# Kernel optimization log

Measured on AMD Instinct MI355X. Metric: run time of the kernel, lower is better.

The kernel has to match this reference:

```python
import jax, jax.numpy as jnp
import numpy as np

Z_NUM_LIST = [[1,1]]*12 + [[2,1]] + [[2,2]]*11 + [[4,2]] + [[4,4]]*11  # 36 layers
Z_DIM, IN_SZ, OUT_SZ, FS = 64, 16, 16, 3
N_Z = sum(o*i for o, i in Z_NUM_LIST)  # 242
_OFFS = np.concatenate([[0], np.cumsum([o*i for o, i in Z_NUM_LIST])]).astype(int)
BN_EPS = 1e-5


def setup_inputs() -> dict:
    key = jax.random.key(0)
    ks = jax.random.split(key, 8)
    x = jax.random.normal(ks[0], (1024, 3, 32, 32), dtype=jnp.float32)
    conv_w = jax.random.normal(ks[1], (16, 3, 3, 3), dtype=jnp.float32) * 0.1
    conv_b = jnp.zeros((16,), dtype=jnp.float32)
    bn_gamma = jnp.ones((16,), dtype=jnp.float32)
    bn_beta = jnp.zeros((16,), dtype=jnp.float32)
    z_all = jax.random.normal(ks[2], (N_Z, Z_DIM), dtype=jnp.float32)  # 242 z-vectors
    # HyperNet params: z -> (in_sz*z_dim), reshape (in_sz, z_dim), -> (in_sz, out_sz*f*f)
    w2 = jax.random.normal(ks[3], (Z_DIM, IN_SZ * Z_DIM), dtype=jnp.float32) * 0.125
    b2 = jnp.zeros((IN_SZ * Z_DIM,), dtype=jnp.float32)
    w1 = jax.random.normal(ks[4], (Z_DIM, OUT_SZ * FS * FS), dtype=jnp.float32) * 0.125
    b1 = jnp.zeros((OUT_SZ * FS * FS,), dtype=jnp.float32)
    return {"x": x, "conv_w": conv_w, "conv_b": conv_b, "bn_gamma": bn_gamma,
            "bn_beta": bn_beta, "z_all": z_all, "w1": w1, "b1": b1, "w2": w2, "b2": b2}


def _hypernet_batched(z_all, w1, b1, w2, b2):
    # All 242 tiny per-z MLPs as one stacked GEMM pair.
    h_in = (z_all @ w2 + b2).reshape(-1, IN_SZ, Z_DIM)          # [N, 16, 64]
    h_fin = jnp.einsum('nid,do->nio', h_in, w1) + b1            # [N, 16, 144]
    return h_fin.reshape(-1, OUT_SZ, IN_SZ, FS, FS)             # torch .view semantics


def _assemble_weights(kernels):
    # Replicates nested torch.cat(dim=1) then cat(dim=0) per Embedding.
    weights = []
    for li, (o_n, i_n) in enumerate(Z_NUM_LIST):
        k = kernels[_OFFS[li]:_OFFS[li + 1]].reshape(o_n, i_n, OUT_SZ, IN_SZ, FS, FS)
        w = k.transpose(0, 2, 1, 3, 4, 5).reshape(o_n * OUT_SZ, i_n * IN_SZ, FS, FS)
        weights.append(w)
    return weights


def reference(x, conv_w, conv_b, bn_gamma, bn_beta, z_all, w1, b1, w2, b2):
    # conv1 (3->16, 3x3, pad 1)
    y = jax.lax.conv_general_dilated(x, conv_w, (1, 1), 'SAME',
                                     dimension_numbers=('NCHW', 'OIHW', 'NCHW'))
    y = y + conv_b[None, :, None, None]
    # batchnorm (training mode: batch statistics) + relu
    mean = jnp.mean(y, axis=(0, 2, 3))
    var = jnp.var(y, axis=(0, 2, 3))
    y = (y - mean[None, :, None, None]) * jax.lax.rsqrt(var + BN_EPS)[None, :, None, None]
    y = jax.nn.relu(y * bn_gamma[None, :, None, None] + bn_beta[None, :, None, None])
    # hypernetwork weight generation (36 conv weight tensors)
    kernels = _hypernet_batched(z_all, w1, b1, w2, b2)
    weights = _assemble_weights(kernels)
    return (*weights, y)
```

## Files before the change

### kernel.cpp

```cpp
#include <hip/hip_runtime.h>

#define N_Z     242
#define W_ELEMS (N_Z * 2304)
#define NHW_F   1048576.0f

__constant__ int c_offs[37] = {0,1,2,3,4,5,6,7,8,9,10,11,12,14,18,22,26,30,34,38,
                               42,46,50,54,58,66,82,98,114,130,146,162,178,194,210,226,242};
__constant__ int c_isz[36] = {1,1,1,1,1,1,1,1,1,1,1,1, 1, 2,2,2,2,2,2,2,2,2,2,2, 2,
                              4,4,4,4,4,4,4,4,4,4,4};

template<int CTRL, int RMASK>
__device__ __forceinline__ float dpp_add(float x) {
    int s = __builtin_amdgcn_update_dpp(0, __float_as_int(x), CTRL, RMASK, 0xF, true);
    return x + __int_as_float(s);
}
__device__ __forceinline__ float wave_sum64(float x) {
    x = dpp_add<0x111, 0xF>(x);
    x = dpp_add<0x112, 0xF>(x);
    x = dpp_add<0x114, 0xF>(x);
    x = dpp_add<0x118, 0xF>(x);
    x = dpp_add<0x142, 0xA>(x);
    x = dpp_add<0x143, 0xC>(x);
    return x;
}

__device__ __forceinline__ void stage_x(const float* __restrict__ xp,
                                        float (*xs)[34][35], int t)
{
    for (int idx = t; idx < 3 * 34 * 35; idx += 256) {
        const int ci  = idx / 1190;
        const int rem = idx - ci * 1190;
        const int rr  = rem / 35, cc = rem - rr * 35;
        float v = 0.0f;
        if (rr >= 1 && rr <= 32 && cc >= 1 && cc <= 32)
            v = xp[ci * 1024 + (rr - 1) * 32 + (cc - 1)];
        xs[ci][rr][cc] = v;
    }
}

__device__ __forceinline__ void load_window(const float (*xs)[34][35],
                                            float xv[3][3][6], int h, int w0)
{
    #pragma unroll
    for (int ci = 0; ci < 3; ++ci)
        #pragma unroll
        for (int rr = 0; rr < 3; ++rr)
            #pragma unroll
            for (int j = 0; j < 6; ++j)
                xv[ci][rr][j] = xs[ci][h + rr][w0 + j];
}

union Smem1 {
    struct { float zsh[64]; float hin[1024]; } h;
    struct { float xs[3][34][35]; float red[4][32]; } c;
};

__global__ __launch_bounds__(256, 4) void fused_hyper_stats(
    const float* __restrict__ x,     const float* __restrict__ cw,
    const float* __restrict__ cb,
    const float* __restrict__ z_all, const float* __restrict__ w1,
    const float* __restrict__ b1,    const float* __restrict__ w2,
    const float* __restrict__ b2,    float* __restrict__ out,
    float* __restrict__ gacc)
{
    __shared__ Smem1 sm;
    const int t = threadIdx.x;

    if (blockIdx.x < N_Z) {
        const int n = blockIdx.x;
        if (t < 64) sm.h.zsh[t] = z_all[n * 64 + t];
        __syncthreads();

        float4 a = *(const float4*)(b2 + 4 * t);
        for (int e = 0; e < 64; ++e) {
            const float zv = sm.h.zsh[e];
            const float4 wr = *(const float4*)(w2 + e * 1024 + 4 * t);
            a.x += zv * wr.x; a.y += zv * wr.y; a.z += zv * wr.z; a.w += zv * wr.w;
        }
        *(float4*)(sm.h.hin + 4 * t) = a;
        __syncthreads();

        int li = 0;
        while (n >= c_offs[li + 1]) ++li;
        const int r   = n - c_offs[li];
        const int isz = c_isz[li];
        const int sh  = isz >> 1;
        const int o   = r >> sh;
        const int ii  = r & (isz - 1);
        float* wout = out + (long)c_offs[li] * 2304;

        const int aI = t >> 4, q = t & 15;
        float acc[9];
        #pragma unroll
        for (int j = 0; j < 9; ++j) acc[j] = b1[9 * q + j];
        const float* __restrict__ hp = sm.h.hin + aI * 64;
        const float* __restrict__ wp = w1 + 9 * q;
        #pragma unroll 4
        for (int d = 0; d < 64; ++d) {
            const float hv = hp[d];
            #pragma unroll
            for (int j = 0; j < 9; ++j) acc[j] += hv * wp[d * 144 + j];
        }
        float* op = wout + (o * 16 + aI) * (isz * 144) + (ii * 16 + q) * 9;
        #pragma unroll
        for (int j = 0; j < 9; ++j) op[j] = acc[j];
    } else {
        const int n = blockIdx.x - N_Z;
        stage_x(x + n * 3072, sm.c.xs, t);
        __syncthreads();

        const int h = t >> 3, w0 = (t & 7) << 2;
        float xv[3][3][6];
        load_window(sm.c.xs, xv, h, w0);

        const int lane = t & 63, wid = t >> 6;
        const int wl = (lane < 27) ? lane : (lane < 54 ? lane - 27 : 0);

        #pragma unroll
        for (int co = 0; co < 16; ++co) {
            const float wlv = cw[co * 27 + wl];
            float w[27];
            #pragma unroll
            for (int k = 0; k < 27; ++k)
                w[k] = __int_as_float(__builtin_amdgcn_readlane(__float_as_int(wlv), k));

            const float bias = cb[co];
            float a0 = bias, a1 = bias, a2 = bias, a3 = bias;
            #pragma unroll
            for (int ci = 0; ci < 3; ++ci)
                #pragma unroll
                for (int rr = 0; rr < 3; ++rr) {
                    const int kb = ci * 9 + rr * 3;
                    a0 += w[kb] * xv[ci][rr][0] + w[kb+1] * xv[ci][rr][1] + w[kb+2] * xv[ci][rr][2];
                    a1 += w[kb] * xv[ci][rr][1] + w[kb+1] * xv[ci][rr][2] + w[kb+2] * xv[ci][rr][3];
                    a2 += w[kb] * xv[ci][rr][2] + w[kb+1] * xv[ci][rr][3] + w[kb+2] * xv[ci][rr][4];
                    a3 += w[kb] * xv[ci][rr][3] + w[kb+1] * xv[ci][rr][4] + w[kb+2] * xv[ci][rr][5];
                }
            float s = wave_sum64(a0 + a1 + a2 + a3);
            float qv = wave_sum64(a0 * a0 + a1 * a1 + a2 * a2 + a3 * a3);
            if (lane == 63) {
                sm.c.red[wid][co]      = s;
                sm.c.red[wid][16 + co] = qv;
            }
        }
        __syncthreads();
        if (t < 32) {
            const float v = sm.c.red[0][t] + sm.c.red[1][t] +
                            sm.c.red[2][t] + sm.c.red[3][t];
            atomicAdd(&gacc[(n & 7) * 32 + t], v);
        }
    }
}

__global__ __launch_bounds__(256, 4) void conv_bn_relu_kernel(
    const float* __restrict__ x,    const float* __restrict__ cw,
    const float* __restrict__ cb,   const float* __restrict__ gacc,
    const float* __restrict__ gamma,const float* __restrict__ beta,
    float* __restrict__ y)
{
    __shared__ float xs[3][34][35];
    __shared__ float ssh[32];
    const int n = blockIdx.x, t = threadIdx.x;

    stage_x(x + n * 3072, xs, t);
    if (t < 16) {
        float S = 0.0f, Q = 0.0f;
        #pragma unroll
        for (int k = 0; k < 8; ++k) {
            S += gacc[k * 32 + t];
            Q += gacc[k * 32 + 16 + t];
        }
        const float inv  = 1.0f / NHW_F;
        const float mean = S * inv;
        const float var  = Q * inv - mean * mean;
        const float rs   = rsqrtf(var + 1e-5f);
        const float sc   = gamma[t] * rs;
        ssh[2 * t]     = sc;
        ssh[2 * t + 1] = beta[t] - mean * sc;
    }
    __syncthreads();

    const int h = t >> 3, w0 = (t & 7) << 2;
    float xv[3][3][6];
    load_window(xs, xv, h, w0);

    const int lane = t & 63;
    const int wl = (lane < 27) ? lane : (lane < 54 ? lane - 27 : 0);

    float* yp = y + n * 16384;
    #pragma unroll
    for (int co = 0; co < 16; ++co) {
        const float wlv = cw[co * 27 + wl];
        float w[27];
        #pragma unroll
        for (int k = 0; k < 27; ++k)
            w[k] = __int_as_float(__builtin_amdgcn_readlane(__float_as_int(wlv), k));

        const float bias = cb[co];
        float a0 = bias, a1 = bias, a2 = bias, a3 = bias;
        #pragma unroll
        for (int ci = 0; ci < 3; ++ci)
            #pragma unroll
            for (int rr = 0; rr < 3; ++rr) {
                const int kb = ci * 9 + rr * 3;
                a0 += w[kb] * xv[ci][rr][0] + w[kb+1] * xv[ci][rr][1] + w[kb+2] * xv[ci][rr][2];
                a1 += w[kb] * xv[ci][rr][1] + w[kb+1] * xv[ci][rr][2] + w[kb+2] * xv[ci][rr][3];
                a2 += w[kb] * xv[ci][rr][2] + w[kb+1] * xv[ci][rr][3] + w[kb+2] * xv[ci][rr][4];
                a3 += w[kb] * xv[ci][rr][3] + w[kb+1] * xv[ci][rr][4] + w[kb+2] * xv[ci][rr][5];
            }
        const float sc = ssh[2 * co], sf = ssh[2 * co + 1];
        float4 o4;
        o4.x = fmaxf(0.0f, a0 * sc + sf);
        o4.y = fmaxf(0.0f, a1 * sc + sf);
        o4.z = fmaxf(0.0f, a2 * sc + sf);
        o4.w = fmaxf(0.0f, a3 * sc + sf);
        *(float4*)(yp + co * 1024 + h * 32 + w0) = o4;
    }
}

extern "C" void kernel_launch(void* const* d_in, const int* in_sizes, int n_in,
                              void* d_out, int out_size, void* d_ws, size_t ws_size,
                              hipStream_t stream)
{
    const float* x     = (const float*)d_in[0];
    const float* cw    = (const float*)d_in[1];
    const float* cb    = (const float*)d_in[2];
    const float* gamma = (const float*)d_in[3];
    const float* beta  = (const float*)d_in[4];
    const float* z_all = (const float*)d_in[5];
    const float* w1    = (const float*)d_in[6];
    const float* b1    = (const float*)d_in[7];
    const float* w2    = (const float*)d_in[8];
    const float* b2    = (const float*)d_in[9];

    float* out  = (float*)d_out;
    float* gacc = (float*)d_ws;
    float* y    = out + W_ELEMS;

    fused_hyper_stats<<<N_Z + 1024, 256, 0, stream>>>(x, cw, cb, z_all, w1, b1, w2, b2,
                                                      out, gacc);
    conv_bn_relu_kernel<<<1024, 256, 0, stream>>>(x, cw, cb, gacc, gamma, beta, y);
}
```

Before: 152.6 us.

## Fuse conv stats, hypernet, and BN-ReLU into one cooperative grid-synced kernel

Replaces the two-kernel sequence with a single cooperative kernel of 512 blocks. Each block handles two images, keeps the conv outputs in registers across a grid.sync, and applies BN+ReLU afterwards, so the second pass no longer recomputes the convolution or reloads x. Hypernet blocks now stage w1 in shared memory and run their work before the grid sync. Conv weights are read as scalar loads instead of readlane broadcasts. The risks are higher register pressure from 128 accumulators per thread, a reduced occupancy bound, and whether cooperative launch succeeds. If it fails, the code falls back to the old two-kernel path.

```diff
diff --git a/kernel.cpp b/kernel.cpp
--- a/kernel.cpp
+++ b/kernel.cpp
@@ -1,8 +1,12 @@
 #include <hip/hip_runtime.h>
+#include <hip/hip_cooperative_groups.h>
+
+namespace cg = cooperative_groups;
 
 #define N_Z     242
 #define W_ELEMS (N_Z * 2304)
 #define NHW_F   1048576.0f
+#define NBLK    512
 
 __constant__ int c_offs[37] = {0,1,2,3,4,5,6,7,8,9,10,11,12,14,18,22,26,30,34,38,
                                42,46,50,54,58,66,82,98,114,130,146,162,178,194,210,226,242};
@@ -50,34 +54,91 @@
                 xv[ci][rr][j] = xs[ci][h + rr][w0 + j];
 }
 
-union Smem1 {
-    struct { float zsh[64]; float hin[1024]; } h;
-    struct { float xs[3][34][35]; float red[4][32]; } c;
+union SmemU {
+    float xs[2][3][34][35];
+    struct { float w1s[64 * 144]; float zsh[64]; float hin[1024]; } h;
 };
 
-__global__ __launch_bounds__(256, 4) void fused_hyper_stats(
+__global__ __launch_bounds__(256, 2) void mega_kernel(
     const float* __restrict__ x,     const float* __restrict__ cw,
-    const float* __restrict__ cb,
-    const float* __restrict__ z_all, const float* __restrict__ w1,
-    const float* __restrict__ b1,    const float* __restrict__ w2,
-    const float* __restrict__ b2,    float* __restrict__ out,
-    float* __restrict__ gacc)
-{
-    __shared__ Smem1 sm;
-    const int t = threadIdx.x;
-
-    if (blockIdx.x < N_Z) {
-        const int n = blockIdx.x;
-        if (t < 64) sm.h.zsh[t] = z_all[n * 64 + t];
+    const float* __restrict__ cb,    const float* __restrict__ gamma,
+    const float* __restrict__ beta,  const float* __restrict__ z_all,
+    const float* __restrict__ w1,    const float* __restrict__ b1,
+    const float* __restrict__ w2,    const float* __restrict__ b2,
+    float* __restrict__ out,         float* __restrict__ gacc,
+    float* __restrict__ y)
+{
+    __shared__ SmemU smu;
+    __shared__ float red[4][32];
+    __shared__ float ssh[32];
+
+    const int b = blockIdx.x, t = threadIdx.x;
+    const int lane = t & 63, wid = t >> 6;
+    cg::grid_group grid = cg::this_grid();
+
+    stage_x(x + (2 * b) * 3072,     smu.xs[0], t);
+    stage_x(x + (2 * b + 1) * 3072, smu.xs[1], t);
+    __syncthreads();
+
+    const int h = t >> 3, w0 = (t & 7) << 2;
+    float acc[2][16][4];
+
+    #pragma unroll
+    for (int img = 0; img < 2; ++img) {
+        float xv[3][3][6];
+        load_window(smu.xs[img], xv, h, w0);
+        #pragma unroll
+        for (int co = 0; co < 16; ++co) {
+            const float bias = cb[co];
+            float a0 = bias, a1 = bias, a2 = bias, a3 = bias;
+            #pragma unroll
+            for (int ci = 0; ci < 3; ++ci)
+                #pragma unroll
+                for (int rr = 0; rr < 3; ++rr) {
+                    const float wA = cw[co * 27 + ci * 9 + rr * 3 + 0];
+                    const float wB = cw[co * 27 + ci * 9 + rr * 3 + 1];
+                    const float wC = cw[co * 27 + ci * 9 + rr * 3 + 2];
+                    a0 += wA * xv[ci][rr][0] + wB * xv[ci][rr][1] + wC * xv[ci][rr][2];
+                    a1 += wA * xv[ci][rr][1] + wB * xv[ci][rr][2] + wC * xv[ci][rr][3];
+                    a2 += wA * xv[ci][rr][2] + wB * xv[ci][rr][3] + wC * xv[ci][rr][4];
+                    a3 += wA * xv[ci][rr][3] + wB * xv[ci][rr][4] + wC * xv[ci][rr][5];
+                }
+            acc[img][co][0] = a0; acc[img][co][1] = a1;
+            acc[img][co][2] = a2; acc[img][co][3] = a3;
+        }
+    }
+    #pragma unroll
+    for (int co = 0; co < 16; ++co) {
+        float s = 0.0f, q = 0.0f;
+        #pragma unroll
+        for (int img = 0; img < 2; ++img)
+            #pragma unroll
+            for (int j = 0; j < 4; ++j) {
+                const float v = acc[img][co][j];
+                s += v; q += v * v;
+            }
+        s = wave_sum64(s); q = wave_sum64(q);
+        if (lane == 63) { red[wid][co] = s; red[wid][16 + co] = q; }
+    }
+    __syncthreads();
+    if (t < 32) {
+        const float v = red[0][t] + red[1][t] + red[2][t] + red[3][t];
+        atomicAdd(&gacc[(b & 7) * 32 + t], v);
+    }
+
+    if (b < N_Z) {
+        const int n = b;
+        if (t < 64) smu.h.zsh[t] = z_all[n * 64 + t];
+        for (int i = t; i < 64 * 144; i += 256) smu.h.w1s[i] = w1[i];
         __syncthreads();
 
         float4 a = *(const float4*)(b2 + 4 * t);
         for (int e = 0; e < 64; ++e) {
-            const float zv = sm.h.zsh[e];
+            const float zv = smu.h.zsh[e];
             const float4 wr = *(const float4*)(w2 + e * 1024 + 4 * t);
             a.x += zv * wr.x; a.y += zv * wr.y; a.z += zv * wr.z; a.w += zv * wr.w;
         }
-        *(float4*)(sm.h.hin + 4 * t) = a;
+        *(float4*)(smu.h.hin + 4 * t) = a;
         __syncthreads();
 
         int li = 0;
@@ -90,79 +151,24 @@
         float* wout = out + (long)c_offs[li] * 2304;
 
         const int aI = t >> 4, q = t & 15;
-        float acc[9];
-        #pragma unroll
-        for (int j = 0; j < 9; ++j) acc[j] = b1[9 * q + j];
-        const float* __restrict__ hp = sm.h.hin + aI * 64;
-        const float* __restrict__ wp = w1 + 9 * q;
+        float hacc[9];
+        #pragma unroll
+        for (int j = 0; j < 9; ++j) hacc[j] = b1[9 * q + j];
+        const float* hp = smu.h.hin + aI * 64;
+        const float* wp = smu.h.w1s + 9 * q;
         #pragma unroll 4
         for (int d = 0; d < 64; ++d) {
             const float hv = hp[d];
             #pragma unroll
-            for (int j = 0; j < 9; ++j) acc[j] += hv * wp[d * 144 + j];
+            for (int j = 0; j < 9; ++j) hacc[j] += hv * wp[d * 144 + j];
         }
         float* op = wout + (o * 16 + aI) * (isz * 144) + (ii * 16 + q) * 9;
         #pragma unroll
-        for (int j = 0; j < 9; ++j) op[j] = acc[j];
-    } else {
-        const int n = blockIdx.x - N_Z;
-        stage_x(x + n * 3072, sm.c.xs, t);
-        __syncthreads();
-
-        const int h = t >> 3, w0 = (t & 7) << 2;
-        float xv[3][3][6];
-        load_window(sm.c.xs, xv, h, w0);
-
-        const int lane = t & 63, wid = t >> 6;
-        const int wl = (lane < 27) ? lane : (lane < 54 ? lane - 27 : 0);
-
-        #pragma unroll
-        for (int co = 0; co < 16; ++co) {
-            const float wlv = cw[co * 27 + wl];
-            float w[27];
-            #pragma unroll
-            for (int k = 0; k < 27; ++k)
-                w[k] = __int_as_float(__builtin_amdgcn_readlane(__float_as_int(wlv), k));
-
-            const float bias = cb[co];
-            float a0 = bias, a1 = bias, a2 = bias, a3 = bias;
-            #pragma unroll
-            for (int ci = 0; ci < 3; ++ci)
-                #pragma unroll
-                for (int rr = 0; rr < 3; ++rr) {
-                    const int kb = ci * 9 + rr * 3;
-                    a0 += w[kb] * xv[ci][rr][0] + w[kb+1] * xv[ci][rr][1] + w[kb+2] * xv[ci][rr][2];
-                    a1 += w[kb] * xv[ci][rr][1] + w[kb+1] * xv[ci][rr][2] + w[kb+2] * xv[ci][rr][3];
-                    a2 += w[kb] * xv[ci][rr][2] + w[kb+1] * xv[ci][rr][3] + w[kb+2] * xv[ci][rr][4];
-                    a3 += w[kb] * xv[ci][rr][3] + w[kb+1] * xv[ci][rr][4] + w[kb+2] * xv[ci][rr][5];
-                }
-            float s = wave_sum64(a0 + a1 + a2 + a3);
-            float qv = wave_sum64(a0 * a0 + a1 * a1 + a2 * a2 + a3 * a3);
-            if (lane == 63) {
-                sm.c.red[wid][co]      = s;
-                sm.c.red[wid][16 + co] = qv;
-            }
-        }
-        __syncthreads();
-        if (t < 32) {
-            const float v = sm.c.red[0][t] + sm.c.red[1][t] +
-                            sm.c.red[2][t] + sm.c.red[3][t];
-            atomicAdd(&gacc[(n & 7) * 32 + t], v);
-        }
-    }
-}
-
-__global__ __launch_bounds__(256, 4) void conv_bn_relu_kernel(
-    const float* __restrict__ x,    const float* __restrict__ cw,
-    const float* __restrict__ cb,   const float* __restrict__ gacc,
-    const float* __restrict__ gamma,const float* __restrict__ beta,
-    float* __restrict__ y)
-{
-    __shared__ float xs[3][34][35];
-    __shared__ float ssh[32];
-    const int n = blockIdx.x, t = threadIdx.x;
-
-    stage_x(x + n * 3072, xs, t);
+        for (int j = 0; j < 9; ++j) op[j] = hacc[j];
+    }
+
+    grid.sync();
+
     if (t < 16) {
         float S = 0.0f, Q = 0.0f;
         #pragma unroll
@@ -180,33 +186,162 @@
     }
     __syncthreads();
 
+    #pragma unroll
+    for (int img = 0; img < 2; ++img) {
+        float* yp = y + (long)(2 * b + img) * 16384;
+        #pragma unroll
+        for (int co = 0; co < 16; ++co) {
+            const float sc = ssh[2 * co], sf = ssh[2 * co + 1];
+            float4 o4;
+            o4.x = fmaxf(0.0f, acc[img][co][0] * sc + sf);
+            o4.y = fmaxf(0.0f, acc[img][co][1] * sc + sf);
+            o4.z = fmaxf(0.0f, acc[img][co][2] * sc + sf);
+            o4.w = fmaxf(0.0f, acc[img][co][3] * sc + sf);
+            *(float4*)(yp + co * 1024 + h * 32 + w0) = o4;
+        }
+    }
+}
+
+union Smem1 {
+    struct { float zsh[64]; float hin[1024]; } h;
+    struct { float xs[3][34][35]; float red[4][32]; } c;
+};
+
+__global__ __launch_bounds__(256, 4) void fused_hyper_stats(
+    const float* __restrict__ x,     const float* __restrict__ cw,
+    const float* __restrict__ cb,
+    const float* __restrict__ z_all, const float* __restrict__ w1,
+    const float* __restrict__ b1,    const float* __restrict__ w2,
+    const float* __restrict__ b2,    float* __restrict__ out,
+    float* __restrict__ gacc)
+{
+    __shared__ Smem1 sm;
+    const int t = threadIdx.x;
+
+    if (blockIdx.x < N_Z) {
+        const int n = blockIdx.x;
+        if (t < 64) sm.h.zsh[t] = z_all[n * 64 + t];
+        __syncthreads();
+        float4 a = *(const float4*)(b2 + 4 * t);
+        for (int e = 0; e < 64; ++e) {
+            const float zv = sm.h.zsh[e];
+            const float4 wr = *(const float4*)(w2 + e * 1024 + 4 * t);
+            a.x += zv * wr.x; a.y += zv * wr.y; a.z += zv * wr.z; a.w += zv * wr.w;
+        }
+        *(float4*)(sm.h.hin + 4 * t) = a;
+        __syncthreads();
+
+        int li = 0;
+        while (n >= c_offs[li + 1]) ++li;
+        const int r   = n - c_offs[li];
+        const int isz = c_isz[li];
+        const int sh  = isz >> 1;
+        const int o   = r >> sh;
+        const int ii  = r & (isz - 1);
+        float* wout = out + (long)c_offs[li] * 2304;
+
+        const int aI = t >> 4, q = t & 15;
+        float acc[9];
+        #pragma unroll
+        for (int j = 0; j < 9; ++j) acc[j] = b1[9 * q + j];
+        const float* hp = sm.h.hin + aI * 64;
+        const float* wp = w1 + 9 * q;
+        #pragma unroll 4
+        for (int d = 0; d < 64; ++d) {
+            const float hv = hp[d];
+            #pragma unroll
+            for (int j = 0; j < 9; ++j) acc[j] += hv * wp[d * 144 + j];
+        }
+        float* op = wout + (o * 16 + aI) * (isz * 144) + (ii * 16 + q) * 9;
+        #pragma unroll
+        for (int j = 0; j < 9; ++j) op[j] = acc[j];
+    } else {
+        const int n = blockIdx.x - N_Z;
+        stage_x(x + n * 3072, sm.c.xs, t);
+        __syncthreads();
+
+        const int h = t >> 3, w0 = (t & 7) << 2;
+        float xv[3][3][6];
+        load_window(sm.c.xs, xv, h, w0);
+
+        const int lane = t & 63, wid = t >> 6;
+        #pragma unroll
+        for (int co = 0; co < 16; ++co) {
+            const float bias = cb[co];
+            float a0 = bias, a1 = bias, a2 = bias, a3 = bias;
+            #pragma unroll
+            for (int ci = 0; ci < 3; ++ci)
+                #pragma unroll
+                for (int rr = 0; rr < 3; ++rr) {
+                    const float wA = cw[co * 27 + ci * 9 + rr * 3 + 0];
+                    const float wB = cw[co * 27 + ci * 9 + rr * 3 + 1];
+                    const float wC = cw[co * 27 + ci * 9 + rr * 3 + 2];
+                    a0 += wA * xv[ci][rr][0] + wB * xv[ci][rr][1] + wC * xv[ci][rr][2];
+                    a1 += wA * xv[ci][rr][1] + wB * xv[ci][rr][2] + wC * xv[ci][rr][3];
+                    a2 += wA * xv[ci][rr][2] + wB * xv[ci][rr][3] + wC * xv[ci][rr][4];
+                    a3 += wA * xv[ci][rr][3] + wB * xv[ci][rr][4] + wC * xv[ci][rr][5];
+                }
+            float s = wave_sum64(a0 + a1 + a2 + a3);
+            float qv = wave_sum64(a0 * a0 + a1 * a1 + a2 * a2 + a3 * a3);
+            if (lane == 63) { sm.c.red[wid][co] = s; sm.c.red[wid][16 + co] = qv; }
+        }
+        __syncthreads();
+        if (t < 32) {
+            const float v = sm.c.red[0][t] + sm.c.red[1][t] +
+                            sm.c.red[2][t] + sm.c.red[3][t];
+            atomicAdd(&gacc[(n & 7) * 32 + t], v);
+        }
+    }
+}
+
+__global__ __launch_bounds__(256, 4) void conv_bn_relu_kernel(
+    const float* __restrict__ x,    const float* __restrict__ cw,
+    const float* __restrict__ cb,   const float* __restrict__ gacc,
+    const float* __restrict__ gamma,const float* __restrict__ beta,
+    float* __restrict__ y)
+{
+    __shared__ float xs[3][34][35];
+    __shared__ float ssh[32];
+    const int n = blockIdx.x, t = threadIdx.x;
+
+    stage_x(x + n * 3072, xs, t);
+    if (t < 16) {
+        float S = 0.0f, Q = 0.0f;
+        #pragma unroll
+        for (int k = 0; k < 8; ++k) {
+            S += gacc[k * 32 + t];
+            Q += gacc[k * 32 + 16 + t];
+        }
+        const float inv  = 1.0f / NHW_F;
+        const float mean = S * inv;
+        const float var  = Q * inv - mean * mean;
+        const float rs   = rsqrtf(var + 1e-5f);
+        const float sc   = gamma[t] * rs;
+        ssh[2 * t]     = sc;
+        ssh[2 * t + 1] = beta[t] - mean * sc;
+    }
+    __syncthreads();
+
     const int h = t >> 3, w0 = (t & 7) << 2;
     float xv[3][3][6];
     load_window(xs, xv, h, w0);
 
-    const int lane = t & 63;
-    const int wl = (lane < 27) ? lane : (lane < 54 ? lane - 27 : 0);
-
     float* yp = y + n * 16384;
     #pragma unroll
     for (int co = 0; co < 16; ++co) {
-        const float wlv = cw[co * 27 + wl];
-        float w[27];
-        #pragma unroll
-        for (int k = 0; k < 27; ++k)
-            w[k] = __int_as_float(__builtin_amdgcn_readlane(__float_as_int(wlv), k));
-
         const float bias = cb[co];
         float a0 = bias, a1 = bias, a2 = bias, a3 = bias;
         #pragma unroll
         for (int ci = 0; ci < 3; ++ci)
             #pragma unroll
             for (int rr = 0; rr < 3; ++rr) {
-                const int kb = ci * 9 + rr * 3;
-                a0 += w[kb] * xv[ci][rr][0] + w[kb+1] * xv[ci][rr][1] + w[kb+2] * xv[ci][rr][2];
-                a1 += w[kb] * xv[ci][rr][1] + w[kb+1] * xv[ci][rr][2] + w[kb+2] * xv[ci][rr][3];
-                a2 += w[kb] * xv[ci][rr][2] + w[kb+1] * xv[ci][rr][3] + w[kb+2] * xv[ci][rr][4];
-                a3 += w[kb] * xv[ci][rr][3] + w[kb+1] * xv[ci][rr][4] + w[kb+2] * xv[ci][rr][5];
+                const float wA = cw[co * 27 + ci * 9 + rr * 3 + 0];
+                const float wB = cw[co * 27 + ci * 9 + rr * 3 + 1];
+                const float wC = cw[co * 27 + ci * 9 + rr * 3 + 2];
+                a0 += wA * xv[ci][rr][0] + wB * xv[ci][rr][1] + wC * xv[ci][rr][2];
+                a1 += wA * xv[ci][rr][1] + wB * xv[ci][rr][2] + wC * xv[ci][rr][3];
+                a2 += wA * xv[ci][rr][2] + wB * xv[ci][rr][3] + wC * xv[ci][rr][4];
+                a3 += wA * xv[ci][rr][3] + wB * xv[ci][rr][4] + wC * xv[ci][rr][5];
             }
         const float sc = ssh[2 * co], sf = ssh[2 * co + 1];
         float4 o4;
@@ -237,7 +372,14 @@
     float* gacc = (float*)d_ws;
     float* y    = out + W_ELEMS;
 
-    fused_hyper_stats<<<N_Z + 1024, 256, 0, stream>>>(x, cw, cb, z_all, w1, b1, w2, b2,
-                                                      out, gacc);
-    conv_bn_relu_kernel<<<1024, 256, 0, stream>>>(x, cw, cb, gacc, gamma, beta, y);
-}
+    void* args[] = {(void*)&x, (void*)&cw, (void*)&cb, (void*)&gamma, (void*)&beta,
+                    (void*)&z_all, (void*)&w1, (void*)&b1, (void*)&w2, (void*)&b2,
+                    (void*)&out, (void*)&gacc, (void*)&y};
+    hipError_t err = hipLaunchCooperativeKernel((void*)mega_kernel, dim3(NBLK),
+                                                dim3(256), args, 0, stream);
+    if (err != hipSuccess) {
+        fused_hyper_stats<<<N_Z + 1024, 256, 0, stream>>>(x, cw, cb, z_all, w1, b1,
+                                                          w2, b2, out, gacc);
+        conv_bn_relu_kernel<<<1024, 256, 0, stream>>>(x, cw, cb, gacc, gamma, beta, y);
+    }
+}
```

Result: slower. 211.2 us (+38.4%).
